# Kernel optimization log

Measured on AMD Instinct MI355X. Metric: run time of the kernel, lower is better.

The kernel has to match this reference:

```python
import jax, jax.numpy as jnp
import numpy as np
from jax import lax

NUM_GROUP = 512    # G: number of FPS centers
GROUP_SIZE = 32    # M: KNN neighbors per center


def setup_inputs() -> dict:
    key = jax.random.key(0)
    xyz = jax.random.normal(key, (32, 8192, 3), dtype=jnp.float32)  # B N 3
    return {"xyz": xyz}


def _fps(xyz, num_group):
    """Iterative farthest point sampling. xyz: [B,N,3] -> idx [B,G] int32.
    Deterministic start at point 0 (matching pointnet2-style fps)."""
    B, N, _ = xyz.shape

    def step(carry, _):
        dists, last_idx = carry                       # dists: [B,N] running min sq-dist
        last = xyz[jnp.arange(B), last_idx]           # [B,3] most recent center
        d = jnp.sum((xyz - last[:, None, :]) ** 2, axis=-1)  # [B,N]
        dists = jnp.minimum(dists, d)
        nxt = jnp.argmax(dists, axis=-1).astype(jnp.int32)   # farthest point
        return (dists, nxt), nxt

    init_idx = jnp.zeros((B,), jnp.int32)
    init_d = jnp.full((B, N), jnp.inf, xyz.dtype)
    (_, _), idxs = lax.scan(step, (init_d, init_idx), None, length=num_group - 1)
    return jnp.concatenate([init_idx[None, :], idxs], axis=0).T  # [B,G]


def reference(xyz):
    B, N, _ = xyz.shape
    G, M = NUM_GROUP, GROUP_SIZE

    fps_idx = _fps(xyz, G)                              # [B,G] int32
    center = xyz[jnp.arange(B)[:, None], fps_idx]       # [B,G,3]

    # KNN: for each center, k nearest points in xyz (squared euclidean)
    # dist2[b,g,n] = |c|^2 + |x|^2 - 2 c.x   -> [B,G,N]
    x2 = jnp.sum(xyz * xyz, axis=-1)                    # [B,N]
    c2 = jnp.sum(center * center, axis=-1)              # [B,G]
    dist2 = c2[:, :, None] + x2[:, None, :] - 2.0 * jnp.einsum('bgd,bnd->bgn', center, xyz)
    _, idx = lax.top_k(-dist2, M)                       # [B,G,M] nearest-first

    neighborhood = xyz[jnp.arange(B)[:, None, None], idx]   # [B,G,M,3]
    neighborhood = neighborhood - center[:, :, None, :]
    return neighborhood, center, fps_idx
```

## Files before the change

kernel.cpp:

```cpp
#include <hip/hip_runtime.h>
#include <math.h>

#define BATCH  32
#define NPTS   8192
#define NGROUP 512
#define MSIZE  32

#define FPS_THREADS 512
#define SXYZ_FLOATS (NPTS * 3)
#define DYN_LDS_BYTES (SXYZ_FLOATS * 4)

typedef float v2f __attribute__((ext_vector_type(2)));

template<int CTRL>
__device__ __forceinline__ float dpp_max_f32(float x) {
    int o = __builtin_amdgcn_update_dpp(0, __float_as_int(x), CTRL, 0xF, 0xF, true);
    float f = __int_as_float(o);
    return x > f ? x : f;
}
template<int CTRL>
__device__ __forceinline__ unsigned dpp_min_u32_full(unsigned x) {
    unsigned o = (unsigned)__builtin_amdgcn_update_dpp(0, (int)x, CTRL, 0xF, 0xF, true);
    return o < x ? o : x;
}

__global__ __launch_bounds__(FPS_THREADS, 2)
void fps_kernel(const float* __restrict__ xyz,
                float* __restrict__ out_center,
                float* __restrict__ out_fps)
{
#pragma clang fp contract(off)
    extern __shared__ float sxyz[];
    __shared__ unsigned long long gkey[3];

    const int b    = blockIdx.x;
    const int t    = threadIdx.x;
    const int lane = t & 63;
    const float* bp = xyz + (size_t)b * NPTS * 3;
    const float4* bp4 = reinterpret_cast<const float4*>(bp);
    float4* s4 = reinterpret_cast<float4*>(sxyz);

    v2f px2[8], py2[8], pz2[8], dist2[8];
    {
        float f[48];
        #pragma unroll
        for (int q = 0; q < 12; ++q) {
            float4 v = bp4[t * 12 + q];
            s4[t * 12 + q] = v;
            f[q*4+0] = v.x; f[q*4+1] = v.y; f[q*4+2] = v.z; f[q*4+3] = v.w;
        }
        #pragma unroll
        for (int j = 0; j < 8; ++j) {
            px2[j] = (v2f){f[6*j+0], f[6*j+3]};
            py2[j] = (v2f){f[6*j+1], f[6*j+4]};
            pz2[j] = (v2f){f[6*j+2], f[6*j+5]};
            dist2[j] = (v2f){INFINITY, INFINITY};
        }
    }
    if (t == 0) { gkey[0] = 0; gkey[1] = 0; gkey[2] = 0; }
    __syncthreads();

    if (t == 0) {
        out_fps[(size_t)b * NGROUP] = 0.0f;
        out_center[(size_t)(b * NGROUP) * 3 + 0] = sxyz[0];
        out_center[(size_t)(b * NGROUP) * 3 + 1] = sxyz[1];
        out_center[(size_t)(b * NGROUP) * 3 + 2] = sxyz[2];
    }

    int last = 0;
    for (int g = 1; g < NGROUP; ++g) {
        const int slot = g % 3;
        const int nxt  = (g + 1) % 3;
        float lx = sxyz[last*3 + 0];
        float ly = sxyz[last*3 + 1];
        float lz = sxyz[last*3 + 2];

        #pragma unroll
        for (int j = 0; j < 8; ++j) {
            v2f dx = px2[j] - lx;
            v2f dy = py2[j] - ly;
            v2f dz = pz2[j] - lz;
            v2f t1 = dx * dx;
            v2f t2 = dy * dy;
            v2f t3 = dz * dz;
            v2f s  = t1 + t2;
            v2f d  = s + t3;
            dist2[j] = __builtin_elementwise_min(dist2[j], d);
        }
        v2f mm0 = __builtin_elementwise_max(dist2[0], dist2[1]);
        v2f mm1 = __builtin_elementwise_max(dist2[2], dist2[3]);
        v2f mm2 = __builtin_elementwise_max(dist2[4], dist2[5]);
        v2f mm3 = __builtin_elementwise_max(dist2[6], dist2[7]);
        v2f mma = __builtin_elementwise_max(mm0, mm1);
        v2f mmb = __builtin_elementwise_max(mm2, mm3);
        v2f mmc = __builtin_elementwise_max(mma, mmb);
        float m_t = fmaxf(mmc.x, mmc.y);

        float m = m_t;
        m = dpp_max_f32<0xB1>(m);
        m = dpp_max_f32<0x4E>(m);
        m = dpp_max_f32<0x141>(m);
        m = dpp_max_f32<0x140>(m);
        m = dpp_max_f32<0x142>(m);
        m = dpp_max_f32<0x143>(m);
        float wmax = __int_as_float(__builtin_amdgcn_readlane(__float_as_int(m), 63));

        unsigned long long mask = __ballot(m_t == wmax);
        int l = __ffsll((long long)mask) - 1;

        unsigned lj = 0;
        #pragma unroll
        for (int j = 15; j >= 0; --j) {
            float dj = (j & 1) ? dist2[j >> 1].y : dist2[j >> 1].x;
            lj = (dj == wmax) ? (unsigned)j : lj;
        }
        unsigned idx = ((unsigned)t << 4) | lj;
        unsigned widx = (unsigned)__builtin_amdgcn_readlane((int)idx, l);

        if (lane == 63) {
            unsigned long long key =
                (((unsigned long long)__float_as_uint(wmax)) << 32) | (unsigned)~widx;
            atomicMax(&gkey[slot], key);
            if (t == 63) gkey[nxt] = 0;
        }
        __syncthreads();

        unsigned long long kq = gkey[slot];
        int fi = (int)(~(unsigned)kq);
        last = fi;
        if (t == 0) {
            out_fps[(size_t)b * NGROUP + g] = (float)fi;
            out_center[((size_t)(b * NGROUP + g)) * 3 + 0] = sxyz[fi*3 + 0];
            out_center[((size_t)(b * NGROUP + g)) * 3 + 1] = sxyz[fi*3 + 1];
            out_center[((size_t)(b * NGROUP + g)) * 3 + 2] = sxyz[fi*3 + 2];
        }
    }
}

__global__ __launch_bounds__(256)
void knn_kernel(const float* __restrict__ xyz,
                const float* __restrict__ center,
                float* __restrict__ out_nbhd)
{
    const int lane = threadIdx.x & 63;
    const int gid  = blockIdx.x * 4 + (threadIdx.x >> 6);
    const int b    = gid >> 9;
    const float* bp = xyz + (size_t)b * NPTS * 3;
    const float4* bp4 = reinterpret_cast<const float4*>(bp);

    const float cx = center[(size_t)gid*3+0];
    const float cy = center[(size_t)gid*3+1];
    const float cz = center[(size_t)gid*3+2];

    unsigned kl[4];
    #pragma unroll
    for (int k = 0; k < 4; ++k) kl[k] = 0xFFFFFFFFu;

    for (int c = 0; c < 32; ++c) {
        int f4 = c * 192 + lane * 3;
        float4 a  = bp4[f4+0];
        float4 bq = bp4[f4+1];
        float4 cq = bp4[f4+2];
        unsigned p0 = (unsigned)(c * 256 + lane * 4);
        v2f xA = (v2f){a.x,  a.w},  yA = (v2f){a.y,  bq.x}, zA = (v2f){a.z,  bq.y};
        v2f xB = (v2f){bq.z, cq.y}, yB = (v2f){bq.w, cq.z}, zB = (v2f){cq.x, cq.w};
        v2f dxA = xA - cx, dyA = yA - cy, dzA = zA - cz;
        v2f dxB = xB - cx, dyB = yB - cy, dzB = zB - cz;
        v2f dA = dxA*dxA + dyA*dyA + dzA*dzA;
        v2f dB = dxB*dxB + dyB*dyB + dzB*dzB;
        float ds[4] = {dA.x, dA.y, dB.x, dB.y};
        #pragma unroll
        for (int k = 0; k < 4; ++k) {
            unsigned key = (__float_as_uint(ds[k]) & 0xFFFFE000u) | (p0 + k);
            if (key < kl[3]) {
                kl[3] = key;
                #pragma unroll
                for (int q = 3; q > 0; --q) {
                    if (kl[q] < kl[q-1]) {
                        unsigned tk = kl[q]; kl[q] = kl[q-1]; kl[q-1] = tk;
                    }
                }
            }
        }
    }

    int keep = 0;
    #pragma unroll 1
    for (int r = 0; r < MSIZE; ++r) {
        unsigned k = kl[0];
        k = dpp_min_u32_full<0xB1>(k);
        k = dpp_min_u32_full<0x4E>(k);
        k = dpp_min_u32_full<0x141>(k);
        k = dpp_min_u32_full<0x140>(k);
        {
            unsigned o = __shfl_xor(k, 16);
            k = o < k ? o : k;
            o = __shfl_xor(k, 32);
            k = o < k ? o : k;
        }
        if (lane == r) keep = (int)(k & 0x1FFFu);
        if (kl[0] == k) {
            kl[0] = kl[1]; kl[1] = kl[2]; kl[2] = kl[3];
            kl[3] = 0xFFFFFFFFu;
        }
    }

    if (lane < MSIZE) {
        size_t o = ((size_t)gid * MSIZE + lane) * 3;
        float x = bp[keep*3+0], y = bp[keep*3+1], z = bp[keep*3+2];
        out_nbhd[o+0] = x - cx;
        out_nbhd[o+1] = y - cy;
        out_nbhd[o+2] = z - cz;
    }
}

extern "C" void kernel_launch(void* const* d_in, const int* in_sizes, int n_in,
                              void* d_out, int out_size, void* d_ws, size_t ws_size,
                              hipStream_t stream)
{
    const float* xyz = (const float*)d_in[0];
    float* out        = (float*)d_out;
    float* out_nbhd   = out;
    float* out_center = out + (size_t)BATCH*NGROUP*MSIZE*3;
    float* out_fps    = out_center + (size_t)BATCH*NGROUP*3;

    hipFuncSetAttribute(reinterpret_cast<const void*>(fps_kernel),
                        hipFuncAttributeMaxDynamicSharedMemorySize,
                        DYN_LDS_BYTES);

    fps_kernel<<<dim3(BATCH), dim3(FPS_THREADS), DYN_LDS_BYTES, stream>>>(xyz, out_center, out_fps);
    knn_kernel<<<dim3(BATCH*NGROUP/4), dim3(256), 0, stream>>>(xyz, out_center, out_nbhd);
}
```

Baseline: 576.7 us.

## Replace FPS LDS atomic reduction with per-wave slots and DPP cross-wave max

In the FPS kernel each wave now writes its best (distance, index) key to a double-buffered per-wave LDS slot. After the barrier every wave reduces the eight slots with 64-bit DPP max, which replaces the shared atomicMax and the three-slot reset scheme. Point coordinates are stored as padded float4 in LDS so the winning center is fetched with a single load, and the KNN selection uses a full DPP row reduction plus readlane instead of shuffles. It also unrolls the KNN scan loop; the padded layout costs extra LDS (128KB) and may reduce occupancy.

```diff
diff --git a/kernel.cpp b/kernel.cpp
--- a/kernel.cpp
+++ b/kernel.cpp
@@ -7,8 +7,7 @@
 #define MSIZE  32
 
 #define FPS_THREADS 512
-#define SXYZ_FLOATS (NPTS * 3)
-#define DYN_LDS_BYTES (SXYZ_FLOATS * 4)
+#define DYN_LDS_BYTES (NPTS * 16)
 
 typedef float v2f __attribute__((ext_vector_type(2)));
 
@@ -19,9 +18,16 @@
     return x > f ? x : f;
 }
 template<int CTRL>
-__device__ __forceinline__ unsigned dpp_min_u32_full(unsigned x) {
-    unsigned o = (unsigned)__builtin_amdgcn_update_dpp(0, (int)x, CTRL, 0xF, 0xF, true);
+__device__ __forceinline__ unsigned dpp_min_u32_keep(unsigned x) {
+    unsigned o = (unsigned)__builtin_amdgcn_update_dpp((int)x, (int)x, CTRL, 0xF, 0xF, false);
     return o < x ? o : x;
+}
+template<int CTRL>
+__device__ __forceinline__ unsigned long long dpp_max_u64(unsigned long long k) {
+    int lo2 = __builtin_amdgcn_update_dpp(0, (int)(unsigned)k,        CTRL, 0xF, 0xF, true);
+    int hi2 = __builtin_amdgcn_update_dpp(0, (int)(unsigned)(k >> 32), CTRL, 0xF, 0xF, true);
+    unsigned long long k2 = (((unsigned long long)(unsigned)hi2) << 32) | (unsigned)lo2;
+    return k2 > k ? k2 : k;
 }
 
 __global__ __launch_bounds__(FPS_THREADS, 2)
@@ -30,15 +36,15 @@
                 float* __restrict__ out_fps)
 {
 #pragma clang fp contract(off)
-    extern __shared__ float sxyz[];
-    __shared__ unsigned long long gkey[3];
+    extern __shared__ float4 sxyz4[];
+    __shared__ unsigned long long wkey[2][8];
 
     const int b    = blockIdx.x;
     const int t    = threadIdx.x;
     const int lane = t & 63;
+    const int wid  = t >> 6;
     const float* bp = xyz + (size_t)b * NPTS * 3;
     const float4* bp4 = reinterpret_cast<const float4*>(bp);
-    float4* s4 = reinterpret_cast<float4*>(sxyz);
 
     v2f px2[8], py2[8], pz2[8], dist2[8];
     {
@@ -46,9 +52,11 @@
         #pragma unroll
         for (int q = 0; q < 12; ++q) {
             float4 v = bp4[t * 12 + q];
-            s4[t * 12 + q] = v;
             f[q*4+0] = v.x; f[q*4+1] = v.y; f[q*4+2] = v.z; f[q*4+3] = v.w;
         }
+        #pragma unroll
+        for (int k = 0; k < 16; ++k)
+            sxyz4[t * 16 + k] = make_float4(f[3*k+0], f[3*k+1], f[3*k+2], 0.0f);
         #pragma unroll
         for (int j = 0; j < 8; ++j) {
             px2[j] = (v2f){f[6*j+0], f[6*j+3]};
@@ -57,23 +65,18 @@
             dist2[j] = (v2f){INFINITY, INFINITY};
         }
     }
-    if (t == 0) { gkey[0] = 0; gkey[1] = 0; gkey[2] = 0; }
     __syncthreads();
 
     if (t == 0) {
         out_fps[(size_t)b * NGROUP] = 0.0f;
-        out_center[(size_t)(b * NGROUP) * 3 + 0] = sxyz[0];
-        out_center[(size_t)(b * NGROUP) * 3 + 1] = sxyz[1];
-        out_center[(size_t)(b * NGROUP) * 3 + 2] = sxyz[2];
-    }
-
-    int last = 0;
+        out_center[(size_t)(b * NGROUP) * 3 + 0] = bp[0];
+        out_center[(size_t)(b * NGROUP) * 3 + 1] = bp[1];
+        out_center[(size_t)(b * NGROUP) * 3 + 2] = bp[2];
+    }
+
+    float lx = sxyz4[0].x, ly = sxyz4[0].y, lz = sxyz4[0].z;
     for (int g = 1; g < NGROUP; ++g) {
-        const int slot = g % 3;
-        const int nxt  = (g + 1) % 3;
-        float lx = sxyz[last*3 + 0];
-        float ly = sxyz[last*3 + 1];
-        float lz = sxyz[last*3 + 2];
+        const int p = g & 1;
 
         #pragma unroll
         for (int j = 0; j < 8; ++j) {
@@ -118,21 +121,24 @@
         unsigned widx = (unsigned)__builtin_amdgcn_readlane((int)idx, l);
 
         if (lane == 63) {
-            unsigned long long key =
+            wkey[p][wid] =
                 (((unsigned long long)__float_as_uint(wmax)) << 32) | (unsigned)~widx;
-            atomicMax(&gkey[slot], key);
-            if (t == 63) gkey[nxt] = 0;
         }
         __syncthreads();
 
-        unsigned long long kq = gkey[slot];
+        unsigned long long kq = wkey[p][lane & 7];
+        kq = dpp_max_u64<0xB1>(kq);
+        kq = dpp_max_u64<0x4E>(kq);
+        kq = dpp_max_u64<0x141>(kq);
         int fi = (int)(~(unsigned)kq);
-        last = fi;
+
+        float4 wc = sxyz4[fi];
+        lx = wc.x; ly = wc.y; lz = wc.z;
         if (t == 0) {
             out_fps[(size_t)b * NGROUP + g] = (float)fi;
-            out_center[((size_t)(b * NGROUP + g)) * 3 + 0] = sxyz[fi*3 + 0];
-            out_center[((size_t)(b * NGROUP + g)) * 3 + 1] = sxyz[fi*3 + 1];
-            out_center[((size_t)(b * NGROUP + g)) * 3 + 2] = sxyz[fi*3 + 2];
+            out_center[((size_t)(b * NGROUP + g)) * 3 + 0] = wc.x;
+            out_center[((size_t)(b * NGROUP + g)) * 3 + 1] = wc.y;
+            out_center[((size_t)(b * NGROUP + g)) * 3 + 2] = wc.z;
         }
     }
 }
@@ -156,6 +162,7 @@
     #pragma unroll
     for (int k = 0; k < 4; ++k) kl[k] = 0xFFFFFFFFu;
 
+    #pragma unroll 4
     for (int c = 0; c < 32; ++c) {
         int f4 = c * 192 + lane * 3;
         float4 a  = bp4[f4+0];
@@ -188,18 +195,15 @@
     #pragma unroll 1
     for (int r = 0; r < MSIZE; ++r) {
         unsigned k = kl[0];
-        k = dpp_min_u32_full<0xB1>(k);
-        k = dpp_min_u32_full<0x4E>(k);
-        k = dpp_min_u32_full<0x141>(k);
-        k = dpp_min_u32_full<0x140>(k);
-        {
-            unsigned o = __shfl_xor(k, 16);
-            k = o < k ? o : k;
-            o = __shfl_xor(k, 32);
-            k = o < k ? o : k;
-        }
-        if (lane == r) keep = (int)(k & 0x1FFFu);
-        if (kl[0] == k) {
+        k = dpp_min_u32_keep<0xB1>(k);
+        k = dpp_min_u32_keep<0x4E>(k);
+        k = dpp_min_u32_keep<0x141>(k);
+        k = dpp_min_u32_keep<0x140>(k);
+        k = dpp_min_u32_keep<0x142>(k);
+        k = dpp_min_u32_keep<0x143>(k);
+        unsigned kmin = (unsigned)__builtin_amdgcn_readlane((int)k, 63);
+        if (lane == r) keep = (int)(kmin & 0x1FFFu);
+        if (kl[0] == kmin) {
             kl[0] = kl[1]; kl[1] = kl[2]; kl[2] = kl[3];
             kl[3] = 0xFFFFFFFFu;
         }
```

Result: no change. 587.7 us (+1.9%).

## Process four KNN centers per wavefront with branchless sorting-network insertion

Applied to the files above, without the earlier changes.

Each wavefront in the KNN kernel now handles four centers instead of one, so every loaded point chunk is reused across four distance computations. The data-dependent insert-and-bubble top-4 update becomes a branchless min/max network, and the cross-lane min reduction uses row-broadcast DPP plus readlane instead of shuffles. The four reductions are interleaved to hide latency. The cost is more registers per thread and a quarter as many blocks. The FPS kernel, which probably dominates total time, is unchanged.

```diff
diff --git a/kernel.cpp b/kernel.cpp
--- a/kernel.cpp
+++ b/kernel.cpp
@@ -19,8 +19,8 @@
     return x > f ? x : f;
 }
 template<int CTRL>
-__device__ __forceinline__ unsigned dpp_min_u32_full(unsigned x) {
-    unsigned o = (unsigned)__builtin_amdgcn_update_dpp(0, (int)x, CTRL, 0xF, 0xF, true);
+__device__ __forceinline__ unsigned dpp_min_u32_keep(unsigned x) {
+    unsigned o = (unsigned)__builtin_amdgcn_update_dpp((int)x, (int)x, CTRL, 0xF, 0xF, false);
     return o < x ? o : x;
 }
 
@@ -143,19 +143,27 @@
                 float* __restrict__ out_nbhd)
 {
     const int lane = threadIdx.x & 63;
-    const int gid  = blockIdx.x * 4 + (threadIdx.x >> 6);
-    const int b    = gid >> 9;
+    const int w    = blockIdx.x * 4 + (threadIdx.x >> 6);
+    const int b    = w >> 7;
+    const int g0   = w * 4;
     const float* bp = xyz + (size_t)b * NPTS * 3;
     const float4* bp4 = reinterpret_cast<const float4*>(bp);
 
-    const float cx = center[(size_t)gid*3+0];
-    const float cy = center[(size_t)gid*3+1];
-    const float cz = center[(size_t)gid*3+2];
-
-    unsigned kl[4];
+    float cx[4], cy[4], cz[4];
     #pragma unroll
-    for (int k = 0; k < 4; ++k) kl[k] = 0xFFFFFFFFu;
-
+    for (int k = 0; k < 4; ++k) {
+        cx[k] = center[(size_t)(g0+k)*3+0];
+        cy[k] = center[(size_t)(g0+k)*3+1];
+        cz[k] = center[(size_t)(g0+k)*3+2];
+    }
+
+    unsigned kl[4][4];
+    #pragma unroll
+    for (int k = 0; k < 4; ++k)
+        #pragma unroll
+        for (int q = 0; q < 4; ++q) kl[k][q] = 0xFFFFFFFFu;
+
+    #pragma unroll 2
     for (int c = 0; c < 32; ++c) {
         int f4 = c * 192 + lane * 3;
         float4 a  = bp4[f4+0];
@@ -164,53 +172,66 @@
         unsigned p0 = (unsigned)(c * 256 + lane * 4);
         v2f xA = (v2f){a.x,  a.w},  yA = (v2f){a.y,  bq.x}, zA = (v2f){a.z,  bq.y};
         v2f xB = (v2f){bq.z, cq.y}, yB = (v2f){bq.w, cq.z}, zB = (v2f){cq.x, cq.w};
-        v2f dxA = xA - cx, dyA = yA - cy, dzA = zA - cz;
-        v2f dxB = xB - cx, dyB = yB - cy, dzB = zB - cz;
-        v2f dA = dxA*dxA + dyA*dyA + dzA*dzA;
-        v2f dB = dxB*dxB + dyB*dyB + dzB*dzB;
-        float ds[4] = {dA.x, dA.y, dB.x, dB.y};
         #pragma unroll
         for (int k = 0; k < 4; ++k) {
-            unsigned key = (__float_as_uint(ds[k]) & 0xFFFFE000u) | (p0 + k);
-            if (key < kl[3]) {
-                kl[3] = key;
-                #pragma unroll
-                for (int q = 3; q > 0; --q) {
-                    if (kl[q] < kl[q-1]) {
-                        unsigned tk = kl[q]; kl[q] = kl[q-1]; kl[q-1] = tk;
-                    }
-                }
+            v2f dxA = xA - cx[k], dyA = yA - cy[k], dzA = zA - cz[k];
+            v2f dxB = xB - cx[k], dyB = yB - cy[k], dzB = zB - cz[k];
+            v2f dA = dxA*dxA + dyA*dyA + dzA*dzA;
+            v2f dB = dxB*dxB + dyB*dyB + dzB*dzB;
+            float ds[4] = {dA.x, dA.y, dB.x, dB.y};
+            #pragma unroll
+            for (int e = 0; e < 4; ++e) {
+                unsigned x = (__float_as_uint(ds[e]) & 0xFFFFE000u) | (p0 + e);
+                unsigned m0 = kl[k][0] > x ? kl[k][0] : x;
+                unsigned m1 = kl[k][1] > x ? kl[k][1] : x;
+                unsigned m2 = kl[k][2] > x ? kl[k][2] : x;
+                kl[k][0] = kl[k][0] < x  ? kl[k][0] : x;
+                kl[k][1] = kl[k][1] < m0 ? kl[k][1] : m0;
+                kl[k][2] = kl[k][2] < m1 ? kl[k][2] : m1;
+                kl[k][3] = kl[k][3] < m2 ? kl[k][3] : m2;
             }
         }
     }
 
-    int keep = 0;
+    unsigned keepv[4] = {0u, 0u, 0u, 0u};
     #pragma unroll 1
     for (int r = 0; r < MSIZE; ++r) {
-        unsigned k = kl[0];
-        k = dpp_min_u32_full<0xB1>(k);
-        k = dpp_min_u32_full<0x4E>(k);
-        k = dpp_min_u32_full<0x141>(k);
-        k = dpp_min_u32_full<0x140>(k);
-        {
-            unsigned o = __shfl_xor(k, 16);
-            k = o < k ? o : k;
-            o = __shfl_xor(k, 32);
-            k = o < k ? o : k;
-        }
-        if (lane == r) keep = (int)(k & 0x1FFFu);
-        if (kl[0] == k) {
-            kl[0] = kl[1]; kl[1] = kl[2]; kl[2] = kl[3];
-            kl[3] = 0xFFFFFFFFu;
+        unsigned kk[4];
+        #pragma unroll
+        for (int k = 0; k < 4; ++k) kk[k] = kl[k][0];
+        #pragma unroll
+        for (int k = 0; k < 4; ++k) kk[k] = dpp_min_u32_keep<0xB1>(kk[k]);
+        #pragma unroll
+        for (int k = 0; k < 4; ++k) kk[k] = dpp_min_u32_keep<0x4E>(kk[k]);
+        #pragma unroll
+        for (int k = 0; k < 4; ++k) kk[k] = dpp_min_u32_keep<0x141>(kk[k]);
+        #pragma unroll
+        for (int k = 0; k < 4; ++k) kk[k] = dpp_min_u32_keep<0x140>(kk[k]);
+        #pragma unroll
+        for (int k = 0; k < 4; ++k) kk[k] = dpp_min_u32_keep<0x142>(kk[k]);
+        #pragma unroll
+        for (int k = 0; k < 4; ++k) kk[k] = dpp_min_u32_keep<0x143>(kk[k]);
+        #pragma unroll
+        for (int k = 0; k < 4; ++k) {
+            unsigned kmin = (unsigned)__builtin_amdgcn_readlane((int)kk[k], 63);
+            if (lane == r) keepv[k] = kmin & 0x1FFFu;
+            if (kl[k][0] == kmin) {
+                kl[k][0] = kl[k][1]; kl[k][1] = kl[k][2]; kl[k][2] = kl[k][3];
+                kl[k][3] = 0xFFFFFFFFu;
+            }
         }
     }
 
     if (lane < MSIZE) {
-        size_t o = ((size_t)gid * MSIZE + lane) * 3;
-        float x = bp[keep*3+0], y = bp[keep*3+1], z = bp[keep*3+2];
-        out_nbhd[o+0] = x - cx;
-        out_nbhd[o+1] = y - cy;
-        out_nbhd[o+2] = z - cz;
+        #pragma unroll
+        for (int k = 0; k < 4; ++k) {
+            int keep = (int)keepv[k];
+            size_t o = (((size_t)(g0 + k)) * MSIZE + lane) * 3;
+            float x = bp[keep*3+0], y = bp[keep*3+1], z = bp[keep*3+2];
+            out_nbhd[o+0] = x - cx[k];
+            out_nbhd[o+1] = y - cy[k];
+            out_nbhd[o+2] = z - cz[k];
+        }
     }
 }
 
@@ -229,5 +250,5 @@
                         DYN_LDS_BYTES);
 
     fps_kernel<<<dim3(BATCH), dim3(FPS_THREADS), DYN_LDS_BYTES, stream>>>(xyz, out_center, out_fps);
-    knn_kernel<<<dim3(BATCH*NGROUP/4), dim3(256), 0, stream>>>(xyz, out_center, out_nbhd);
-}
+    knn_kernel<<<dim3(BATCH*NGROUP/16), dim3(256), 0, stream>>>(xyz, out_center, out_nbhd);
+}
```

Result: no change. 582.9 us (+1.1%).
